# Kernel optimization log

Hardware: AMD Instinct MI355X
Metric: run time of the kernel (lower is better)

## Reference

```python
import jax, jax.numpy as jnp
import numpy as np

EPS_NORM = 1e-6
EPS_Q = 1e-5


def rmsnorm(x, g):
    ms = jnp.mean(x * x, axis=-1, keepdims=True)
    return x * jax.lax.rsqrt(ms + EPS_NORM) * g


def bitlinear(x, w, g):
    # RMSNorm -> absmax int8 activation quant -> absmean ternary weight quant -> matmul -> rescale
    xn = rmsnorm(x, g)
    x_scale = jnp.maximum(jnp.max(jnp.abs(xn), axis=-1, keepdims=True), EPS_Q)
    xq = jnp.clip(jnp.round(xn * 127.0 / x_scale), -128.0, 127.0)  # STE irrelevant in fwd
    w_scale = jnp.maximum(jnp.mean(jnp.abs(w)), EPS_Q)
    wq = jnp.clip(jnp.round(w / w_scale), -1.0, 1.0)
    out = jnp.einsum('btd,od->bto', xq, wq)
    return out * (w_scale * x_scale / 127.0)


def rotate_half(x):
    d = x.shape[-1] // 2
    return jnp.concatenate([-x[..., d:], x[..., :d]], axis=-1)


def apply_rope(x, cos, sin):
    # x: [B, H, T, D]; cos/sin: [T, D]
    return x * cos[None, None] + rotate_half(x) * sin[None, None]


def setup_inputs() -> dict:
    key = jax.random.key(0)
    ks = jax.random.split(key, 12)
    B, T, D, H, KV = 2, 2048, 2048, 32, 8
    hd = D // H
    bound = 1.0 / np.sqrt(D)  # ~ kaiming_uniform fan_in
    inp = {
        'x': jax.random.normal(ks[0], (B, T, D), jnp.float32),
        'cos': jax.random.uniform(ks[1], (T, hd), jnp.float32),
        'sin': jax.random.uniform(ks[2], (T, hd), jnp.float32),
        'wq': jax.random.uniform(ks[3], (H * hd, D), jnp.float32, -bound, bound),
        'wk': jax.random.uniform(ks[4], (KV * hd, D), jnp.float32, -bound, bound),
        'wv': jax.random.uniform(ks[5], (KV * hd, D), jnp.float32, -bound, bound),
        'wo': jax.random.uniform(ks[6], (D, H * hd), jnp.float32, -bound, bound),
        'gq': jnp.ones((D,), jnp.float32),
        'gk': jnp.ones((D,), jnp.float32),
        'gv': jnp.ones((D,), jnp.float32),
        'go': jnp.ones((H * hd,), jnp.float32),
    }
    return inp


def reference(x, cos, sin, wq, wk, wv, wo, gq, gk, gv, go):
    B, T, D = x.shape
    H, KV = 32, 8
    hd = D // H
    n_rep = H // KV

    q = bitlinear(x, wq, gq).reshape(B, T, H, hd).transpose(0, 2, 1, 3)   # [B,H,T,hd]
    k = bitlinear(x, wk, gk).reshape(B, T, KV, hd).transpose(0, 2, 1, 3)  # [B,KV,T,hd]
    v = bitlinear(x, wv, gv).reshape(B, T, KV, hd).transpose(0, 2, 1, 3)

    q = apply_rope(q, cos, sin)
    k = apply_rope(k, cos, sin)

    # GQA repeat_interleave on head dim
    k = jnp.repeat(k, n_rep, axis=1)  # [B,H,T,hd]
    v = jnp.repeat(v, n_rep, axis=1)

    scale = 1.0 / np.sqrt(hd)
    scores = jnp.einsum('bhqd,bhkd->bhqk', q, k) * scale
    causal = jnp.tril(jnp.ones((T, T), bool))
    scores = jnp.where(causal, scores, jnp.finfo(scores.dtype).min)
    attn = jax.nn.softmax(scores, axis=-1)
    out = jnp.einsum('bhqk,bhkd->bhqd', attn, v)
    out = out.transpose(0, 2, 1, 3).reshape(B, T, H * hd)
    return bitlinear(out, wo, go)
```

## Files before the change

### kernel.cpp

```cpp
#include <hip/hip_runtime.h>
#include <stdint.h>

constexpr int B   = 2;
constexpr int T   = 2048;
constexpr int D   = 2048;
constexpr int H   = 32;
constexpr int KVH = 8;
constexpr int HD  = 64;
constexpr int R   = B * T;
constexpr int OKV = KVH * HD;

using bf16x8 = __attribute__((ext_vector_type(8))) __bf16;
using f32x4  = __attribute__((ext_vector_type(4))) float;
using i32x4  = __attribute__((ext_vector_type(4))) int;

__device__ inline float fast_exp2(float x) {
#if __has_builtin(__builtin_amdgcn_exp2f)
    return __builtin_amdgcn_exp2f(x);
#else
    return exp2f(x);
#endif
}

__device__ inline float max3f(float a, float b, float c) {
    return fmaxf(fmaxf(a, b), c);
}

__device__ inline uint16_t f2bf(float f) {
    uint32_t u = __float_as_uint(f);
    u += 0x7fff + ((u >> 16) & 1);
    return (uint16_t)(u >> 16);
}

__device__ inline uint32_t pack_bf16(float a, float b) {
#if __has_builtin(__builtin_amdgcn_cvt_pk_bf16_f32)
    union { __attribute__((ext_vector_type(2))) __bf16 v; uint32_t u; } r;
    r.v = __builtin_amdgcn_cvt_pk_bf16_f32(a, b);
    return r.u;
#else
    return (uint32_t)f2bf(a) | ((uint32_t)f2bf(b) << 16);
#endif
}

__device__ inline void async16(const void* g, void* l) {
    __builtin_amdgcn_global_load_lds((const __attribute__((address_space(1))) unsigned int*)g,
                                     (__attribute__((address_space(3))) unsigned int*)l,
                                     16, 0, 0);
}

__global__ void absmean4_kernel(const float* __restrict__ w0, const float* __restrict__ w1,
                                const float* __restrict__ w2, const float* __restrict__ w3,
                                double* __restrict__ sums) {
    __shared__ float red[256];
    const float* ws[4] = {w0, w1, w2, w3};
    const int ns[4] = {D * D, OKV * D, OKV * D, D * D};
    int wi = blockIdx.y;
    const float* w = ws[wi];
    int n = ns[wi];
    int tid = threadIdx.x;
    float s = 0.f;
    for (int i = blockIdx.x * 256 + tid; i < n; i += gridDim.x * 256)
        s += fabsf(w[i]);
    red[tid] = s;
    __syncthreads();
    for (int st = 128; st > 0; st >>= 1) {
        if (tid < st) red[tid] += red[tid + st];
        __syncthreads();
    }
    if (tid == 0) atomicAdd(&sums[wi], (double)red[0]);
}

__global__ void quantw4_kernel(const float* __restrict__ w0, const float* __restrict__ w1,
                               const float* __restrict__ w2, const float* __restrict__ w3,
                               int8_t* __restrict__ o0, int8_t* __restrict__ o1,
                               int8_t* __restrict__ o2, int8_t* __restrict__ o3,
                               const double* __restrict__ sums) {
    const float* ws[4] = {w0, w1, w2, w3};
    int8_t* os[4] = {o0, o1, o2, o3};
    const int ns[4] = {D * D, OKV * D, OKV * D, D * D};
    int wi = blockIdx.y;
    const float* w = ws[wi];
    int8_t* o = os[wi];
    int n = ns[wi];
    float wsc = fmaxf((float)(sums[wi] / (double)n), 1e-5f);
    for (int i = blockIdx.x * 256 + threadIdx.x; i < n; i += gridDim.x * 256) {
        float q = rintf(w[i] / wsc);
        q = fminf(fmaxf(q, -1.f), 1.f);
        o[i] = (int8_t)q;
    }
}

__global__ __launch_bounds__(256) void rmsq3_kernel(const float* __restrict__ X,
        const float* __restrict__ g0, const float* __restrict__ g1, const float* __restrict__ g2,
        int8_t* __restrict__ o0, int8_t* __restrict__ o1, int8_t* __restrict__ o2,
        float* __restrict__ s0, float* __restrict__ s1, float* __restrict__ s2) {
    __shared__ float red[256];
    int row = blockIdx.x, tid = threadIdx.x;
    const float* xr = X + (size_t)row * D;
    float xv[8];
    float ss = 0.f;
#pragma unroll
    for (int i = 0; i < 8; i++) { xv[i] = xr[tid + 256 * i]; ss += xv[i] * xv[i]; }
    red[tid] = ss;
    __syncthreads();
    for (int st = 128; st > 0; st >>= 1) {
        if (tid < st) red[tid] += red[tid + st];
        __syncthreads();
    }
    float rstd = 1.0f / sqrtf(red[0] / (float)D + 1e-6f);

    const float* gs[3] = {g0, g1, g2};
    int8_t* os[3] = {o0, o1, o2};
    float* sc[3] = {s0, s1, s2};
#pragma unroll
    for (int v = 0; v < 3; v++) {
        float xn[8];
        float amax = 0.f;
#pragma unroll
        for (int i = 0; i < 8; i++) {
            xn[i] = xv[i] * rstd * gs[v][tid + 256 * i];
            amax = fmaxf(amax, fabsf(xn[i]));
        }
        __syncthreads();
        red[tid] = amax;
        __syncthreads();
        for (int st = 128; st > 0; st >>= 1) {
            if (tid < st) red[tid] = fmaxf(red[tid], red[tid + st]);
            __syncthreads();
        }
        float xsv = fmaxf(red[0], 1e-5f);
        float q127 = 127.0f / xsv;
#pragma unroll
        for (int i = 0; i < 8; i++) {
            float q = rintf(xn[i] * q127);
            q = fminf(fmaxf(q, -128.f), 127.f);
            os[v][(size_t)row * D + tid + 256 * i] = (int8_t)q;
        }
        if (tid == 0) sc[v][row] = xsv;
    }
}

__global__ __launch_bounds__(256) void rmsq_kernel(const float* __restrict__ X,
                                                   const float* __restrict__ g,
                                                   int8_t* __restrict__ Xq,
                                                   float* __restrict__ xs_out) {
    __shared__ float red[256];
    int row = blockIdx.x, tid = threadIdx.x;
    const float* xr = X + (size_t)row * D;
    float xv[8];
    float ss = 0.f;
#pragma unroll
    for (int i = 0; i < 8; i++) { xv[i] = xr[tid + 256 * i]; ss += xv[i] * xv[i]; }
    red[tid] = ss;
    __syncthreads();
    for (int st = 128; st > 0; st >>= 1) {
        if (tid < st) red[tid] += red[tid + st];
        __syncthreads();
    }
    float rstd = 1.0f / sqrtf(red[0] / (float)D + 1e-6f);

    float xn[8];
    float amax = 0.f;
#pragma unroll
    for (int i = 0; i < 8; i++) {
        xn[i] = xv[i] * rstd * g[tid + 256 * i];
        amax = fmaxf(amax, fabsf(xn[i]));
    }
    __syncthreads();
    red[tid] = amax;
    __syncthreads();
    for (int st = 128; st > 0; st >>= 1) {
        if (tid < st) red[tid] = fmaxf(red[tid], red[tid + st]);
        __syncthreads();
    }
    float xs = fmaxf(red[0], 1e-5f);
    float q127 = 127.0f / xs;
#pragma unroll
    for (int i = 0; i < 8; i++) {
        float q = rintf(xn[i] * q127);
        q = fminf(fmaxf(q, -128.f), 127.f);
        Xq[(size_t)row * D + tid + 256 * i] = (int8_t)q;
    }
    if (tid == 0) xs_out[row] = xs;
}

template<int BN, int MODE>
__global__ __launch_bounds__(256) void gemm_i8_mfma(const int8_t* __restrict__ Xq,
                                                    const int8_t* __restrict__ W8,
                                                    void* __restrict__ outp,
                                                    const float* __restrict__ xs,
                                                    const double* __restrict__ wsum, int wi,
                                                    int nw, int O,
                                                    const float* __restrict__ cs,
                                                    const float* __restrict__ sn) {
    constexpr int NT = BN / 16;
    __shared__ __align__(16) uint8_t As[128 * 128];
    __shared__ __align__(16) uint8_t Bs[BN * 128];

    const int tid  = threadIdx.x;
    const int lane = tid & 63;
    const int wv   = tid >> 6;
    const int n    = lane & 15, quad = lane >> 4;
    const int row0 = blockIdx.y * 128;
    const int col0 = blockIdx.x * BN;

    i32x4 acc[2][NT] = {};

    for (int k0 = 0; k0 < D; k0 += 128) {
        __syncthreads();
#pragma unroll
        for (int j = 0; j < 4; j++) {
            int p = wv * 256 + j * 64 + lane;
            int r = p >> 3, s = p & 7;
            int c = s ^ (r & 7);
            async16(Xq + (size_t)(row0 + r) * D + k0 + c * 16,
                    &As[(size_t)(wv * 256 + j * 64) * 16]);
        }
#pragma unroll
        for (int j = 0; j < BN / 32; j++) {
            int p = wv * (BN * 2) + j * 64 + lane;
            int r = p >> 3, s = p & 7;
            int c = s ^ (r & 7);
            async16(W8 + (size_t)(col0 + r) * D + k0 + c * 16,
                    &Bs[(size_t)(wv * (BN * 2) + j * 64) * 16]);
        }
        __syncthreads();
#pragma unroll
        for (int t = 0; t < 2; t++) {
            i32x4 af[2], bfr[NT];
#pragma unroll
            for (int mt = 0; mt < 2; mt++) {
                int r = wv * 32 + mt * 16 + n;
                af[mt] = *(const i32x4*)&As[r * 128 + (((t * 4 + quad) ^ (r & 7)) * 16)];
            }
#pragma unroll
            for (int nt = 0; nt < NT; nt++) {
                int r = nt * 16 + n;
                bfr[nt] = *(const i32x4*)&Bs[r * 128 + (((t * 4 + quad) ^ (r & 7)) * 16)];
            }
#pragma unroll
            for (int mt = 0; mt < 2; mt++)
#pragma unroll
                for (int nt = 0; nt < NT; nt++)
                    acc[mt][nt] = __builtin_amdgcn_mfma_i32_16x16x64_i8(af[mt], bfr[nt], acc[mt][nt], 0, 0, 0);
        }
    }
    float w = fmaxf((float)(wsum[wi] / (double)nw), 1e-5f);
#pragma unroll
    for (int mt = 0; mt < 2; mt++) {
#pragma unroll
        for (int r2 = 0; r2 < 4; r2++) {
            int row = row0 + wv * 32 + mt * 16 + quad * 4 + r2;
            float f = w * xs[row] * (1.0f / 127.0f);
            if (MODE == 0) {
                float* out = (float*)outp;
#pragma unroll
                for (int nt = 0; nt < NT; nt++)
                    out[(size_t)row * O + col0 + nt * 16 + n] = (float)acc[mt][nt][r2] * f;
            } else {
                uint16_t* out = (uint16_t*)outp;
                int t = row & (T - 1);
#pragma unroll
                for (int nt = 0; nt < NT; nt++) {
                    if ((nt & 3) >= 2) continue;
                    int i = (nt * 16 + n) & 63;
                    float a  = (float)acc[mt][nt][r2] * f;
                    float bb = (float)acc[mt][nt + 2][r2] * f;
                    float c0 = cs[t * HD + i],      s0 = sn[t * HD + i];
                    float c1 = cs[t * HD + i + 32], s1 = sn[t * HD + i + 32];
                    out[(size_t)row * O + col0 + nt * 16 + n]       = f2bf(a * c0 - bb * s0);
                    out[(size_t)row * O + col0 + (nt + 2) * 16 + n] = f2bf(bb * c1 + a * s1);
                }
            }
        }
    }
}

__global__ __launch_bounds__(256) void gemm_kv_mfma(const int8_t* __restrict__ Xv,
                                                    const int8_t* __restrict__ Xk,
                                                    const int8_t* __restrict__ Wv8,
                                                    const int8_t* __restrict__ Wk8,
                                                    uint16_t* __restrict__ vt,
                                                    uint16_t* __restrict__ kout,
                                                    const float* __restrict__ xsv,
                                                    const float* __restrict__ xsk,
                                                    const double* __restrict__ wsum,
                                                    const float* __restrict__ cs,
                                                    const float* __restrict__ sn) {
    constexpr int BN = 64, NT = 4;
    __shared__ __align__(16) uint8_t As[128 * 128];
    __shared__ __align__(16) uint8_t Bs[BN * 128];

    const int z = blockIdx.z;
    const int8_t* Xq = z ? Xk : Xv;
    const int8_t* W8 = z ? Wk8 : Wv8;
    const float* xs  = z ? xsk : xsv;

    const int tid  = threadIdx.x;
    const int lane = tid & 63;
    const int wv   = tid >> 6;
    const int n    = lane & 15, quad = lane >> 4;
    const int row0 = blockIdx.y * 128;
    const int col0 = blockIdx.x * BN;

    i32x4 acc[2][NT] = {};

    for (int k0 = 0; k0 < D; k0 += 128) {
        __syncthreads();
#pragma unroll
        for (int j = 0; j < 4; j++) {
            int p = wv * 256 + j * 64 + lane;
            int r = p >> 3, s = p & 7;
            int c = s ^ (r & 7);
            async16(Xq + (size_t)(row0 + r) * D + k0 + c * 16,
                    &As[(size_t)(wv * 256 + j * 64) * 16]);
        }
#pragma unroll
        for (int j = 0; j < BN / 32; j++) {
            int p = wv * (BN * 2) + j * 64 + lane;
            int r = p >> 3, s = p & 7;
            int c = s ^ (r & 7);
            async16(W8 + (size_t)(col0 + r) * D + k0 + c * 16,
                    &Bs[(size_t)(wv * (BN * 2) + j * 64) * 16]);
        }
        __syncthreads();
#pragma unroll
        for (int t = 0; t < 2; t++) {
            i32x4 af[2], bfr[NT];
#pragma unroll
            for (int mt = 0; mt < 2; mt++) {
                int r = wv * 32 + mt * 16 + n;
                af[mt] = *(const i32x4*)&As[r * 128 + (((t * 4 + quad) ^ (r & 7)) * 16)];
            }
#pragma unroll
            for (int nt = 0; nt < NT; nt++) {
                int r = nt * 16 + n;
                bfr[nt] = *(const i32x4*)&Bs[r * 128 + (((t * 4 + quad) ^ (r & 7)) * 16)];
            }
#pragma unroll
            for (int mt = 0; mt < 2; mt++)
#pragma unroll
                for (int nt = 0; nt < NT; nt++)
                    acc[mt][nt] = __builtin_amdgcn_mfma_i32_16x16x64_i8(af[mt], bfr[nt], acc[mt][nt], 0, 0, 0);
        }
    }
    float w = fmaxf((float)(wsum[z ? 1 : 2] / (double)(OKV * D)), 1e-5f);
    if (z == 0) {
#pragma unroll
        for (int mt = 0; mt < 2; mt++) {
            int rowb = row0 + wv * 32 + mt * 16 + quad * 4;
            int bb = rowb >> 11;
            int tb = rowb & (T - 1);
            float fr[4];
#pragma unroll
            for (int r2 = 0; r2 < 4; r2++)
                fr[r2] = w * xs[rowb + r2] * (1.0f / 127.0f);
#pragma unroll
            for (int nt = 0; nt < NT; nt++) {
                int col = col0 + nt * 16 + n;
                int kvh = col >> 6, d = col & 63;
                uint2 w2;
                w2.x = pack_bf16((float)acc[mt][nt][0] * fr[0], (float)acc[mt][nt][1] * fr[1]);
                w2.y = pack_bf16((float)acc[mt][nt][2] * fr[2], (float)acc[mt][nt][3] * fr[3]);
                *(uint2*)(vt + ((size_t)(bb * KVH + kvh) * 64 + d) * T + tb) = w2;
            }
        }
    } else {
#pragma unroll
        for (int mt = 0; mt < 2; mt++) {
#pragma unroll
            for (int r2 = 0; r2 < 4; r2++) {
                int row = row0 + wv * 32 + mt * 16 + quad * 4 + r2;
                float f = w * xs[row] * (1.0f / 127.0f);
                int t = row & (T - 1);
#pragma unroll
                for (int nt = 0; nt < 2; nt++) {
                    int i = (nt * 16 + n) & 63;
                    float a  = (float)acc[mt][nt][r2] * f;
                    float bb = (float)acc[mt][nt + 2][r2] * f;
                    float c0 = cs[t * HD + i],      s0 = sn[t * HD + i];
                    float c1 = cs[t * HD + i + 32], s1 = sn[t * HD + i + 32];
                    kout[(size_t)row * OKV + col0 + nt * 16 + n]       = f2bf(a * c0 - bb * s0);
                    kout[(size_t)row * OKV + col0 + (nt + 2) * 16 + n] = f2bf(bb * c1 + a * s1);
                }
            }
        }
    }
}

__global__ __launch_bounds__(512, 4) void attn_mfma_kernel(const uint16_t* __restrict__ qh,
                                                           const uint16_t* __restrict__ kh,
                                                           const uint16_t* __restrict__ vt,
                                                           float* __restrict__ out) {
    __shared__ __align__(16) uint16_t KsB[2][64 * 64];
    __shared__ __align__(16) uint16_t VtB[2][64 * 64];
    __shared__ __align__(16) uint16_t Pw[8][16 * 72];

    const int tid  = threadIdx.x;
    const int lane = tid & 63;
    const int wv   = tid >> 6;
    const int p = blockIdx.x, h = blockIdx.y, b = blockIdx.z;
    const int kvh = h >> 2;
    const int n = lane & 15, quad = lane >> 4;
    const float SC = 0.125f * 1.44269504089f;
    const float DEFER = 44.3614f;

    int q_lo[2] = { p * 128 + wv * 16, (15 - p) * 128 + wv * 16 };

    bf16x8 qf[2][2];
#pragma unroll
    for (int i = 0; i < 2; i++) {
        const uint16_t* qp = qh + (size_t)(b * T + q_lo[i] + n) * D + h * HD + quad * 8;
        qf[i][0] = *(const bf16x8*)(qp);
        qf[i][1] = *(const bf16x8*)(qp + 32);
    }

    f32x4 o[2][4] = {};
    float ls[2] = { 0.f, 0.f };
    float m[2] = { -INFINITY, -INFINITY };

    const uint16_t* kbase = kh + (size_t)b * T * OKV + kvh * HD;
    const uint16_t* vbase = vt + (size_t)(b * KVH + kvh) * 64 * T;

    const int nch = 32 - 2 * p;

    {
        int r = tid >> 3, sl = tid & 7;
        int c = sl ^ (r & 7);
        async16(kbase + (size_t)r * OKV + c * 8, &KsB[0][wv * 512]);
        async16(vbase + (size_t)r * T + c * 8,   &VtB[0][wv * 512]);
    }
    __syncthreads();

    for (int ch = 0; ch < nch; ch++) {
        const int cur = ch & 1;
        if (ch + 1 < nch) {
            const int t1 = (ch + 1) * 64;
            int r = tid >> 3, sl = tid & 7;
            int c = sl ^ (r & 7);
            async16(kbase + (size_t)(t1 + r) * OKV + c * 8, &KsB[cur ^ 1][wv * 512]);
            async16(vbase + (size_t)r * T + t1 + c * 8,     &VtB[cur ^ 1][wv * 512]);
        }
        const int t0 = ch * 64;
        const uint16_t* Ks = KsB[cur];
        const uint16_t* Vs = VtB[cur];

#pragma unroll
        for (int i = 0; i < 2; i++) {
            if (t0 > q_lo[i] + 15) continue;
            f32x4 sv[4] = {};
            __builtin_amdgcn_s_setprio(1);
#pragma unroll
            for (int ks = 0; ks < 2; ks++)
#pragma unroll
                for (int mt = 0; mt < 4; mt++) {
                    int r = mt * 16 + n;
                    bf16x8 kfr = *(const bf16x8*)&Ks[r * 64 + (((ks * 4 + quad) ^ (n & 7)) * 8)];
                    sv[mt] = __builtin_amdgcn_mfma_f32_16x16x32_bf16(kfr, qf[i][ks], sv[mt], 0, 0, 0);
                }
            __builtin_amdgcn_s_setprio(0);

            const int qg = q_lo[i] + n;
            const bool diag = (t0 + 63 > q_lo[i]);
            if (diag) {
#pragma unroll
                for (int mt = 0; mt < 4; mt++)
#pragma unroll
                    for (int r2 = 0; r2 < 4; r2++) {
                        int kg = t0 + mt * 16 + quad * 4 + r2;
                        if (kg > qg) sv[mt][r2] = -INFINITY;
                    }
            }
            float r0 = max3f(sv[0][0], sv[0][1], sv[0][2]);
            float r1 = max3f(sv[0][3], sv[1][0], sv[1][1]);
            float r2m = max3f(sv[1][2], sv[1][3], sv[2][0]);
            float r3 = max3f(sv[2][1], sv[2][2], sv[2][3]);
            float r4 = max3f(sv[3][0], sv[3][1], sv[3][2]);
            float mloc = fmaxf(max3f(max3f(r0, r1, r2m), r3, r4), sv[3][3]);
            mloc = fmaxf(mloc, __shfl_xor(mloc, 16));
            mloc = fmaxf(mloc, __shfl_xor(mloc, 32));
            bool upd = (mloc > m[i] + DEFER);
            if (__ballot(upd)) {
                float mnew = fmaxf(m[i], mloc);
                float corr = fast_exp2((m[i] - mnew) * SC);
                m[i] = mnew;
#pragma unroll
                for (int mt = 0; mt < 4; mt++)
#pragma unroll
                    for (int r2 = 0; r2 < 4; r2++) o[i][mt][r2] *= corr;
                ls[i] *= corr;
            }
            float msc = m[i] * SC;
#pragma unroll
            for (int mt = 0; mt < 4; mt++) {
                float pv[4];
#pragma unroll
                for (int r2 = 0; r2 < 4; r2++)
                    pv[r2] = fast_exp2(__builtin_fmaf(sv[mt][r2], SC, -msc));
                ls[i] += (pv[0] + pv[1]) + (pv[2] + pv[3]);
                uint2 w2;
                w2.x = pack_bf16(pv[0], pv[1]);
                w2.y = pack_bf16(pv[2], pv[3]);
                *(uint2*)&Pw[wv][n * 72 + mt * 16 + quad * 4] = w2;
            }
            __builtin_amdgcn_s_setprio(1);
#pragma unroll
            for (int ks = 0; ks < 2; ks++) {
                bf16x8 pf = *(const bf16x8*)&Pw[wv][n * 72 + ks * 32 + quad * 8];
#pragma unroll
                for (int mt = 0; mt < 4; mt++) {
                    int r = mt * 16 + n;
                    bf16x8 vfr = *(const bf16x8*)&Vs[r * 64 + (((ks * 4 + quad) ^ (n & 7)) * 8)];
                    o[i][mt] = __builtin_amdgcn_mfma_f32_16x16x32_bf16(vfr, pf, o[i][mt], 0, 0, 0);
                }
            }
            __builtin_amdgcn_s_setprio(0);
        }
        __syncthreads();
    }

#pragma unroll
    for (int i = 0; i < 2; i++) {
        int qg = q_lo[i] + n;
        float l = ls[i];
        l += __shfl_xor(l, 16);
        l += __shfl_xor(l, 32);
        float inv = 1.0f / l;
#pragma unroll
        for (int mt = 0; mt < 4; mt++) {
            f32x4 ov;
#pragma unroll
            for (int r2 = 0; r2 < 4; r2++) ov[r2] = o[i][mt][r2] * inv;
            *(f32x4*)(out + (size_t)(b * T + qg) * D + h * HD + mt * 16 + quad * 4) = ov;
        }
    }
}

extern "C" void kernel_launch(void* const* d_in, const int* in_sizes, int n_in,
                              void* d_out, int out_size, void* d_ws, size_t ws_size,
                              hipStream_t stream) {
    const float* x   = (const float*)d_in[0];
    const float* cs  = (const float*)d_in[1];
    const float* sn  = (const float*)d_in[2];
    const float* wq  = (const float*)d_in[3];
    const float* wk  = (const float*)d_in[4];
    const float* wv  = (const float*)d_in[5];
    const float* wo  = (const float*)d_in[6];
    const float* gq  = (const float*)d_in[7];
    const float* gk  = (const float*)d_in[8];
    const float* gv  = (const float*)d_in[9];
    const float* go  = (const float*)d_in[10];
    float* out = (float*)d_out;

    uint8_t* w = (uint8_t*)d_ws;
    double* wsum  = (double*)w;
    float* xs     = (float*)(w + 256);
    size_t off = 256 + 4 * (size_t)R * 4;
    int8_t* Wq8 = (int8_t*)(w + off); off += (size_t)D * D;
    int8_t* Wk8 = (int8_t*)(w + off); off += (size_t)OKV * D;
    int8_t* Wv8 = (int8_t*)(w + off); off += (size_t)OKV * D;
    int8_t* Wo8 = (int8_t*)(w + off); off += (size_t)D * D;
    int8_t* Xq_q = (int8_t*)(w + off); off += (size_t)R * D;
    int8_t* Xq_k = (int8_t*)(w + off); off += (size_t)R * D;
    int8_t* Xq_v = (int8_t*)(w + off); off += (size_t)R * D;
    float* ab = (float*)(w + off); off += (size_t)R * D * 4;
    float* vb = (float*)(w + off); off += (size_t)R * OKV * 4;
    uint16_t* qhb = (uint16_t*)(w + off); off += (size_t)R * D * 2;
    uint16_t* vtb = (uint16_t*)vb;
    uint16_t* khb = vtb + (size_t)R * OKV;
    int8_t*   Aq8 = Xq_q;

    (void)hipMemsetAsync(wsum, 0, 64, stream);

    absmean4_kernel<<<dim3(256, 4), 256, 0, stream>>>(wq, wk, wv, wo, wsum);
    quantw4_kernel<<<dim3(1024, 4), 256, 0, stream>>>(wq, wk, wv, wo, Wq8, Wk8, Wv8, Wo8, wsum);

    rmsq3_kernel<<<R, 256, 0, stream>>>(x, gq, gk, gv, Xq_q, Xq_k, Xq_v,
                                        xs + 0 * R, xs + 1 * R, xs + 2 * R);

    gemm_i8_mfma<128, 1><<<dim3(D / 128, R / 128), 256, 0, stream>>>(
        Xq_q, Wq8, qhb, xs + 0 * R, wsum, 0, D * D, D, cs, sn);
    gemm_kv_mfma<<<dim3(OKV / 64, R / 128, 2), 256, 0, stream>>>(
        Xq_v, Xq_k, Wv8, Wk8, vtb, khb, xs + 2 * R, xs + 1 * R, wsum, cs, sn);

    attn_mfma_kernel<<<dim3(8, H, B), 512, 0, stream>>>(qhb, khb, vtb, ab);

    rmsq_kernel<<<R, 256, 0, stream>>>(ab, go, Aq8, xs + 3 * R);
    gemm_i8_mfma<128, 0><<<dim3(D / 128, R / 128), 256, 0, stream>>>(
        Aq8, Wo8, out, xs + 3 * R, wsum, 3, D * D, D, cs, sn);
}
```

Measured before the change: 331.8 us.

## Double-buffer int8 GEMM tiles and split work across eight waves per block

The Q/O and K/V int8 MFMA GEMMs now run 512 threads per block, with each wave owning 16 rows instead of 32. Shared-memory tiles are double-buffered, so the async load of the next K-slice is issued before computing on the current one, with one barrier per iteration instead of two. This aims to hide global-to-LDS latency and raise the number of waves available for latency hiding. In exchange it doubles LDS per block, which can limit resident blocks, and each wave reuses a loaded A fragment across fewer MFMAs.

```diff
diff --git a/kernel.cpp b/kernel.cpp
--- a/kernel.cpp
+++ b/kernel.cpp
@@ -185,17 +185,17 @@
 }
 
 template<int BN, int MODE>
-__global__ __launch_bounds__(256) void gemm_i8_mfma(const int8_t* __restrict__ Xq,
-                                                    const int8_t* __restrict__ W8,
-                                                    void* __restrict__ outp,
-                                                    const float* __restrict__ xs,
-                                                    const double* __restrict__ wsum, int wi,
-                                                    int nw, int O,
-                                                    const float* __restrict__ cs,
-                                                    const float* __restrict__ sn) {
+__global__ __launch_bounds__(512, 4) void gemm_i8_mfma(const int8_t* __restrict__ Xq,
+                                                       const int8_t* __restrict__ W8,
+                                                       void* __restrict__ outp,
+                                                       const float* __restrict__ xs,
+                                                       const double* __restrict__ wsum, int wi,
+                                                       int nw, int O,
+                                                       const float* __restrict__ cs,
+                                                       const float* __restrict__ sn) {
     constexpr int NT = BN / 16;
-    __shared__ __align__(16) uint8_t As[128 * 128];
-    __shared__ __align__(16) uint8_t Bs[BN * 128];
+    __shared__ __align__(16) uint8_t As[2][128 * 128];
+    __shared__ __align__(16) uint8_t Bs[2][BN * 128];
 
     const int tid  = threadIdx.x;
     const int lane = tid & 63;
@@ -204,92 +204,92 @@
     const int row0 = blockIdx.y * 128;
     const int col0 = blockIdx.x * BN;
 
-    i32x4 acc[2][NT] = {};
-
-    for (int k0 = 0; k0 < D; k0 += 128) {
-        __syncthreads();
-#pragma unroll
-        for (int j = 0; j < 4; j++) {
-            int p = wv * 256 + j * 64 + lane;
+    i32x4 acc[NT] = {};
+
+    auto stage = [&](int k0, int buf) {
+#pragma unroll
+        for (int ps = 0; ps < 2; ps++) {
+            int p = ps * 512 + wv * 64 + lane;
             int r = p >> 3, s = p & 7;
             int c = s ^ (r & 7);
             async16(Xq + (size_t)(row0 + r) * D + k0 + c * 16,
-                    &As[(size_t)(wv * 256 + j * 64) * 16]);
-        }
-#pragma unroll
-        for (int j = 0; j < BN / 32; j++) {
-            int p = wv * (BN * 2) + j * 64 + lane;
+                    &As[buf][(ps * 512 + wv * 64) * 16]);
+        }
+#pragma unroll
+        for (int ps = 0; ps < BN / 64; ps++) {
+            int p = ps * 512 + wv * 64 + lane;
             int r = p >> 3, s = p & 7;
             int c = s ^ (r & 7);
             async16(W8 + (size_t)(col0 + r) * D + k0 + c * 16,
-                    &Bs[(size_t)(wv * (BN * 2) + j * 64) * 16]);
-        }
-        __syncthreads();
+                    &Bs[buf][(ps * 512 + wv * 64) * 16]);
+        }
+    };
+
+    stage(0, 0);
+    __syncthreads();
+
+    for (int k0 = 0; k0 < D; k0 += 128) {
+        const int cur = (k0 >> 7) & 1;
+        if (k0 + 128 < D) stage(k0 + 128, cur ^ 1);
 #pragma unroll
         for (int t = 0; t < 2; t++) {
-            i32x4 af[2], bfr[NT];
-#pragma unroll
-            for (int mt = 0; mt < 2; mt++) {
-                int r = wv * 32 + mt * 16 + n;
-                af[mt] = *(const i32x4*)&As[r * 128 + (((t * 4 + quad) ^ (r & 7)) * 16)];
-            }
+            int r = wv * 16 + n;
+            i32x4 af = *(const i32x4*)&As[cur][r * 128 + (((t * 4 + quad) ^ (r & 7)) * 16)];
+            i32x4 bfr[NT];
 #pragma unroll
             for (int nt = 0; nt < NT; nt++) {
-                int r = nt * 16 + n;
-                bfr[nt] = *(const i32x4*)&Bs[r * 128 + (((t * 4 + quad) ^ (r & 7)) * 16)];
-            }
-#pragma unroll
-            for (int mt = 0; mt < 2; mt++)
-#pragma unroll
-                for (int nt = 0; nt < NT; nt++)
-                    acc[mt][nt] = __builtin_amdgcn_mfma_i32_16x16x64_i8(af[mt], bfr[nt], acc[mt][nt], 0, 0, 0);
-        }
-    }
+                int rb = nt * 16 + n;
+                bfr[nt] = *(const i32x4*)&Bs[cur][rb * 128 + (((t * 4 + quad) ^ (rb & 7)) * 16)];
+            }
+#pragma unroll
+            for (int nt = 0; nt < NT; nt++)
+                acc[nt] = __builtin_amdgcn_mfma_i32_16x16x64_i8(af, bfr[nt], acc[nt], 0, 0, 0);
+        }
+        __syncthreads();
+    }
+
     float w = fmaxf((float)(wsum[wi] / (double)nw), 1e-5f);
 #pragma unroll
-    for (int mt = 0; mt < 2; mt++) {
-#pragma unroll
-        for (int r2 = 0; r2 < 4; r2++) {
-            int row = row0 + wv * 32 + mt * 16 + quad * 4 + r2;
-            float f = w * xs[row] * (1.0f / 127.0f);
-            if (MODE == 0) {
-                float* out = (float*)outp;
-#pragma unroll
-                for (int nt = 0; nt < NT; nt++)
-                    out[(size_t)row * O + col0 + nt * 16 + n] = (float)acc[mt][nt][r2] * f;
-            } else {
-                uint16_t* out = (uint16_t*)outp;
-                int t = row & (T - 1);
-#pragma unroll
-                for (int nt = 0; nt < NT; nt++) {
-                    if ((nt & 3) >= 2) continue;
-                    int i = (nt * 16 + n) & 63;
-                    float a  = (float)acc[mt][nt][r2] * f;
-                    float bb = (float)acc[mt][nt + 2][r2] * f;
-                    float c0 = cs[t * HD + i],      s0 = sn[t * HD + i];
-                    float c1 = cs[t * HD + i + 32], s1 = sn[t * HD + i + 32];
-                    out[(size_t)row * O + col0 + nt * 16 + n]       = f2bf(a * c0 - bb * s0);
-                    out[(size_t)row * O + col0 + (nt + 2) * 16 + n] = f2bf(bb * c1 + a * s1);
-                }
-            }
-        }
-    }
-}
-
-__global__ __launch_bounds__(256) void gemm_kv_mfma(const int8_t* __restrict__ Xv,
-                                                    const int8_t* __restrict__ Xk,
-                                                    const int8_t* __restrict__ Wv8,
-                                                    const int8_t* __restrict__ Wk8,
-                                                    uint16_t* __restrict__ vt,
-                                                    uint16_t* __restrict__ kout,
-                                                    const float* __restrict__ xsv,
-                                                    const float* __restrict__ xsk,
-                                                    const double* __restrict__ wsum,
-                                                    const float* __restrict__ cs,
-                                                    const float* __restrict__ sn) {
+    for (int r2 = 0; r2 < 4; r2++) {
+        int row = row0 + wv * 16 + quad * 4 + r2;
+        float f = w * xs[row] * (1.0f / 127.0f);
+        if (MODE == 0) {
+            float* out = (float*)outp;
+#pragma unroll
+            for (int nt = 0; nt < NT; nt++)
+                out[(size_t)row * O + col0 + nt * 16 + n] = (float)acc[nt][r2] * f;
+        } else {
+            uint16_t* out = (uint16_t*)outp;
+            int t = row & (T - 1);
+#pragma unroll
+            for (int nt = 0; nt < NT; nt++) {
+                if ((nt & 3) >= 2) continue;
+                int i = (nt * 16 + n) & 63;
+                float a  = (float)acc[nt][r2] * f;
+                float bb = (float)acc[nt + 2][r2] * f;
+                float c0 = cs[t * HD + i],      s0 = sn[t * HD + i];
+                float c1 = cs[t * HD + i + 32], s1 = sn[t * HD + i + 32];
+                out[(size_t)row * O + col0 + nt * 16 + n]       = f2bf(a * c0 - bb * s0);
+                out[(size_t)row * O + col0 + (nt + 2) * 16 + n] = f2bf(bb * c1 + a * s1);
+            }
+        }
+    }
+}
+
+__global__ __launch_bounds__(512, 4) void gemm_kv_mfma(const int8_t* __restrict__ Xv,
+                                                       const int8_t* __restrict__ Xk,
+                                                       const int8_t* __restrict__ Wv8,
+                                                       const int8_t* __restrict__ Wk8,
+                                                       uint16_t* __restrict__ vt,
+                                                       uint16_t* __restrict__ kout,
+                                                       const float* __restrict__ xsv,
+                                                       const float* __restrict__ xsk,
+                                                       const double* __restrict__ wsum,
+                                                       const float* __restrict__ cs,
+                                                       const float* __restrict__ sn) {
     constexpr int BN = 64, NT = 4;
-    __shared__ __align__(16) uint8_t As[128 * 128];
-    __shared__ __align__(16) uint8_t Bs[BN * 128];
+    __shared__ __align__(16) uint8_t As[2][128 * 128];
+    __shared__ __align__(16) uint8_t Bs[2][BN * 128];
 
     const int z = blockIdx.z;
     const int8_t* Xq = z ? Xk : Xv;
@@ -303,86 +303,82 @@
     const int row0 = blockIdx.y * 128;
     const int col0 = blockIdx.x * BN;
 
-    i32x4 acc[2][NT] = {};
-
-    for (int k0 = 0; k0 < D; k0 += 128) {
-        __syncthreads();
-#pragma unroll
-        for (int j = 0; j < 4; j++) {
-            int p = wv * 256 + j * 64 + lane;
+    i32x4 acc[NT] = {};
+
+    auto stage = [&](int k0, int buf) {
+#pragma unroll
+        for (int ps = 0; ps < 2; ps++) {
+            int p = ps * 512 + wv * 64 + lane;
             int r = p >> 3, s = p & 7;
             int c = s ^ (r & 7);
             async16(Xq + (size_t)(row0 + r) * D + k0 + c * 16,
-                    &As[(size_t)(wv * 256 + j * 64) * 16]);
-        }
-#pragma unroll
-        for (int j = 0; j < BN / 32; j++) {
-            int p = wv * (BN * 2) + j * 64 + lane;
+                    &As[buf][(ps * 512 + wv * 64) * 16]);
+        }
+        {
+            int p = wv * 64 + lane;
             int r = p >> 3, s = p & 7;
             int c = s ^ (r & 7);
             async16(W8 + (size_t)(col0 + r) * D + k0 + c * 16,
-                    &Bs[(size_t)(wv * (BN * 2) + j * 64) * 16]);
-        }
-        __syncthreads();
+                    &Bs[buf][(wv * 64) * 16]);
+        }
+    };
+
+    stage(0, 0);
+    __syncthreads();
+
+    for (int k0 = 0; k0 < D; k0 += 128) {
+        const int cur = (k0 >> 7) & 1;
+        if (k0 + 128 < D) stage(k0 + 128, cur ^ 1);
 #pragma unroll
         for (int t = 0; t < 2; t++) {
-            i32x4 af[2], bfr[NT];
-#pragma unroll
-            for (int mt = 0; mt < 2; mt++) {
-                int r = wv * 32 + mt * 16 + n;
-                af[mt] = *(const i32x4*)&As[r * 128 + (((t * 4 + quad) ^ (r & 7)) * 16)];
-            }
+            int r = wv * 16 + n;
+            i32x4 af = *(const i32x4*)&As[cur][r * 128 + (((t * 4 + quad) ^ (r & 7)) * 16)];
+            i32x4 bfr[NT];
 #pragma unroll
             for (int nt = 0; nt < NT; nt++) {
-                int r = nt * 16 + n;
-                bfr[nt] = *(const i32x4*)&Bs[r * 128 + (((t * 4 + quad) ^ (r & 7)) * 16)];
-            }
-#pragma unroll
-            for (int mt = 0; mt < 2; mt++)
-#pragma unroll
-                for (int nt = 0; nt < NT; nt++)
-                    acc[mt][nt] = __builtin_amdgcn_mfma_i32_16x16x64_i8(af[mt], bfr[nt], acc[mt][nt], 0, 0, 0);
-        }
-    }
+                int rb = nt * 16 + n;
+                bfr[nt] = *(const i32x4*)&Bs[cur][rb * 128 + (((t * 4 + quad) ^ (rb & 7)) * 16)];
+            }
+#pragma unroll
+            for (int nt = 0; nt < NT; nt++)
+                acc[nt] = __builtin_amdgcn_mfma_i32_16x16x64_i8(af, bfr[nt], acc[nt], 0, 0, 0);
+        }
+        __syncthreads();
+    }
+
     float w = fmaxf((float)(wsum[z ? 1 : 2] / (double)(OKV * D)), 1e-5f);
     if (z == 0) {
-#pragma unroll
-        for (int mt = 0; mt < 2; mt++) {
-            int rowb = row0 + wv * 32 + mt * 16 + quad * 4;
-            int bb = rowb >> 11;
-            int tb = rowb & (T - 1);
-            float fr[4];
-#pragma unroll
-            for (int r2 = 0; r2 < 4; r2++)
-                fr[r2] = w * xs[rowb + r2] * (1.0f / 127.0f);
-#pragma unroll
-            for (int nt = 0; nt < NT; nt++) {
-                int col = col0 + nt * 16 + n;
-                int kvh = col >> 6, d = col & 63;
-                uint2 w2;
-                w2.x = pack_bf16((float)acc[mt][nt][0] * fr[0], (float)acc[mt][nt][1] * fr[1]);
-                w2.y = pack_bf16((float)acc[mt][nt][2] * fr[2], (float)acc[mt][nt][3] * fr[3]);
-                *(uint2*)(vt + ((size_t)(bb * KVH + kvh) * 64 + d) * T + tb) = w2;
-            }
+        int rowb = row0 + wv * 16 + quad * 4;
+        int bb = rowb >> 11;
+        int tb = rowb & (T - 1);
+        float fr[4];
+#pragma unroll
+        for (int r2 = 0; r2 < 4; r2++)
+            fr[r2] = w * xs[rowb + r2] * (1.0f / 127.0f);
+#pragma unroll
+        for (int nt = 0; nt < NT; nt++) {
+            int col = col0 + nt * 16 + n;
+            int kvh = col >> 6, d = col & 63;
+            uint2 w2;
+            w2.x = pack_bf16((float)acc[nt][0] * fr[0], (float)acc[nt][1] * fr[1]);
+            w2.y = pack_bf16((float)acc[nt][2] * fr[2], (float)acc[nt][3] * fr[3]);
+            *(uint2*)(vt + ((size_t)(bb * KVH + kvh) * 64 + d) * T + tb) = w2;
         }
     } else {
 #pragma unroll
-        for (int mt = 0; mt < 2; mt++) {
-#pragma unroll
-            for (int r2 = 0; r2 < 4; r2++) {
-                int row = row0 + wv * 32 + mt * 16 + quad * 4 + r2;
-                float f = w * xs[row] * (1.0f / 127.0f);
-                int t = row & (T - 1);
-#pragma unroll
-                for (int nt = 0; nt < 2; nt++) {
-                    int i = (nt * 16 + n) & 63;
-                    float a  = (float)acc[mt][nt][r2] * f;
-                    float bb = (float)acc[mt][nt + 2][r2] * f;
-                    float c0 = cs[t * HD + i],      s0 = sn[t * HD + i];
-                    float c1 = cs[t * HD + i + 32], s1 = sn[t * HD + i + 32];
-                    kout[(size_t)row * OKV + col0 + nt * 16 + n]       = f2bf(a * c0 - bb * s0);
-                    kout[(size_t)row * OKV + col0 + (nt + 2) * 16 + n] = f2bf(bb * c1 + a * s1);
-                }
+        for (int r2 = 0; r2 < 4; r2++) {
+            int row = row0 + wv * 16 + quad * 4 + r2;
+            float f = w * xs[row] * (1.0f / 127.0f);
+            int t = row & (T - 1);
+#pragma unroll
+            for (int nt = 0; nt < 2; nt++) {
+                int i = (nt * 16 + n) & 63;
+                float a  = (float)acc[nt][r2] * f;
+                float bb = (float)acc[nt + 2][r2] * f;
+                float c0 = cs[t * HD + i],      s0 = sn[t * HD + i];
+                float c1 = cs[t * HD + i + 32], s1 = sn[t * HD + i + 32];
+                kout[(size_t)row * OKV + col0 + nt * 16 + n]       = f2bf(a * c0 - bb * s0);
+                kout[(size_t)row * OKV + col0 + (nt + 2) * 16 + n] = f2bf(bb * c1 + a * s1);
             }
         }
     }
@@ -578,14 +574,14 @@
     rmsq3_kernel<<<R, 256, 0, stream>>>(x, gq, gk, gv, Xq_q, Xq_k, Xq_v,
                                         xs + 0 * R, xs + 1 * R, xs + 2 * R);
 
-    gemm_i8_mfma<128, 1><<<dim3(D / 128, R / 128), 256, 0, stream>>>(
+    gemm_i8_mfma<128, 1><<<dim3(D / 128, R / 128), 512, 0, stream>>>(
         Xq_q, Wq8, qhb, xs + 0 * R, wsum, 0, D * D, D, cs, sn);
-    gemm_kv_mfma<<<dim3(OKV / 64, R / 128, 2), 256, 0, stream>>>(
+    gemm_kv_mfma<<<dim3(OKV / 64, R / 128, 2), 512, 0, stream>>>(
         Xq_v, Xq_k, Wv8, Wk8, vtb, khb, xs + 2 * R, xs + 1 * R, wsum, cs, sn);
 
     attn_mfma_kernel<<<dim3(8, H, B), 512, 0, stream>>>(qhb, khb, vtb, ab);
 
     rmsq_kernel<<<R, 256, 0, stream>>>(ab, go, Aq8, xs + 3 * R);
-    gemm_i8_mfma<128, 0><<<dim3(D / 128, R / 128), 256, 0, stream>>>(
+    gemm_i8_mfma<128, 0><<<dim3(D / 128, R / 128), 512, 0, stream>>>(
         Aq8, Wo8, out, xs + 3 * R, wsum, 3, D * D, D, cs, sn);
 }
```

New measurement: 326.9 us. No clear change (-1.5%).
